# Kernel optimization log

Hardware: AMD Instinct MI355X
Metric: run time of the kernel (lower is better)

Reference implementation:

```python
import jax, jax.numpy as jnp
import numpy as np

B, T, F, H, OUT_LEN = 1024, 512, 128, 128, 15


def _lstm_cell(x_t, h, c, Wih, Whh, bih, bhh):
    # PyTorch gate order: i, f, g, o
    gates = x_t @ Wih.T + h @ Whh.T + bih + bhh  # [B, 4H]
    i, f, g, o = jnp.split(gates, 4, axis=-1)
    i = jax.nn.sigmoid(i)
    f = jax.nn.sigmoid(f)
    g = jnp.tanh(g)
    o = jax.nn.sigmoid(o)
    c_new = f * c + i * g
    h_new = o * jnp.tanh(c_new)
    return h_new, c_new


def _lstm_layer(x, Wih, Whh, bih, bhh):
    # x: [B, T, in]; returns (outputs [B,T,H], h_last [B,H], c_last [B,H])
    b = x.shape[0]
    h0 = jnp.zeros((b, Whh.shape[1]), x.dtype)
    c0 = jnp.zeros_like(h0)

    def step(carry, x_t):
        h, c = carry
        h, c = _lstm_cell(x_t, h, c, Wih, Whh, bih, bhh)
        return (h, c), h

    (h_last, c_last), ys = jax.lax.scan(step, (h0, c0), jnp.swapaxes(x, 0, 1))
    return jnp.swapaxes(ys, 0, 1), h_last, c_last


def _forward(x, enc_Wih0, enc_Whh0, enc_bih0, enc_bhh0,
             enc_Wih1, enc_Whh1, enc_bih1, enc_bhh1,
             dec_Wih, dec_Whh, dec_bih, dec_bhh,
             inproj_W, inproj_b, outproj_W, outproj_b, attn_W, attn_b):
    # 2-layer encoder (inter-layer dropout is identity at inference)
    out0, _, _ = _lstm_layer(x, enc_Wih0, enc_Whh0, enc_bih0, enc_bhh0)
    enc_out, h_last, c_last = _lstm_layer(out0, enc_Wih1, enc_Whh1, enc_bih1, enc_bhh1)

    hx, cx = h_last, c_last                       # last layer's final (h, c)
    dec_in = x.mean(axis=1) @ inproj_W.T + inproj_b  # [B, H]
    ctx = enc_out.mean(axis=1)                    # [B, H], same each step

    def dec_step(carry, _):
        h, c, din = carry
        h, c = _lstm_cell(din, h, c, dec_Wih, dec_Whh, dec_bih, dec_bhh)
        h = h + (jnp.concatenate([h, ctx], axis=1) @ attn_W.T + attn_b)
        out = h @ outproj_W.T + outproj_b         # [B, F]
        return (h, c, out), out

    _, outs = jax.lax.scan(dec_step, (hx, cx, dec_in), None, length=OUT_LEN)
    return jnp.swapaxes(outs, 0, 1)               # [B, OUT_LEN, F]


def setup_inputs() -> dict:
    key = jax.random.key(0)
    ks = jax.random.split(key, 20)
    s = 0.05  # small init scale to keep gates unsaturated
    inp = {
        "x": jax.random.normal(ks[0], (B, T, F), jnp.float32),
        "enc_Wih0": jax.random.normal(ks[1], (4 * H, F), jnp.float32) * s,
        "enc_Whh0": jax.random.normal(ks[2], (4 * H, H), jnp.float32) * s,
        "enc_bih0": jax.random.normal(ks[3], (4 * H,), jnp.float32) * s,
        "enc_bhh0": jax.random.normal(ks[4], (4 * H,), jnp.float32) * s,
        "enc_Wih1": jax.random.normal(ks[5], (4 * H, H), jnp.float32) * s,
        "enc_Whh1": jax.random.normal(ks[6], (4 * H, H), jnp.float32) * s,
        "enc_bih1": jax.random.normal(ks[7], (4 * H,), jnp.float32) * s,
        "enc_bhh1": jax.random.normal(ks[8], (4 * H,), jnp.float32) * s,
        "dec_Wih": jax.random.normal(ks[9], (4 * H, H), jnp.float32) * s,
        "dec_Whh": jax.random.normal(ks[10], (4 * H, H), jnp.float32) * s,
        "dec_bih": jax.random.normal(ks[11], (4 * H,), jnp.float32) * s,
        "dec_bhh": jax.random.normal(ks[12], (4 * H,), jnp.float32) * s,
        "inproj_W": jax.random.normal(ks[13], (H, F), jnp.float32) * s,
        "inproj_b": jax.random.normal(ks[14], (H,), jnp.float32) * s,
        "outproj_W": jax.random.normal(ks[15], (F, H), jnp.float32) * s,
        "outproj_b": jax.random.normal(ks[16], (F,), jnp.float32) * s,
        "attn_W": jax.random.normal(ks[17], (H, 2 * H), jnp.float32) * s,
        "attn_b": jax.random.normal(ks[18], (H,), jnp.float32) * s,
    }
    return inp


def reference(x, enc_Wih0, enc_Whh0, enc_bih0, enc_bhh0,
              enc_Wih1, enc_Whh1, enc_bih1, enc_bhh1,
              dec_Wih, dec_Whh, dec_bih, dec_bhh,
              inproj_W, inproj_b, outproj_W, outproj_b, attn_W, attn_b):
    return _forward(x, enc_Wih0, enc_Whh0, enc_bih0, enc_bhh0,
                    enc_Wih1, enc_Whh1, enc_bih1, enc_bhh1,
                    dec_Wih, dec_Whh, dec_bih, dec_bhh,
                    inproj_W, inproj_b, outproj_W, outproj_b, attn_W, attn_b)
```

## Files before the change

### kernel.cpp

```cpp
#include <hip/hip_runtime.h>
#include <cstdint>
#include <cstddef>

#define BDIM 512
#define BB   16
#define T_   512
#define F_   128
#define H_   128
#define B_   1024
#define OUTL 15
#define ASTR 264
#define HSTR 136
#define NBLK 64
#define CHUNK 8

typedef __bf16 bf16_t;
typedef __bf16 bf16x8 __attribute__((ext_vector_type(8)));
typedef float  f32x4  __attribute__((ext_vector_type(4)));

__device__ __forceinline__ float u16tof(unsigned int u) {
    unsigned int v = u << 16;
    return __builtin_bit_cast(float, v);
}

__device__ __forceinline__ float sigm(float x) {
    return __builtin_amdgcn_rcpf(1.0f + __expf(-x));
}
__device__ __forceinline__ float tanh_(float x) {
    float e = __expf(2.0f * x);
    return 1.0f - 2.0f * __builtin_amdgcn_rcpf(e + 1.0f);
}

__device__ __forceinline__ f32x4 mfma16(bf16x8 a, bf16x8 b, f32x4 c) {
    return __builtin_amdgcn_mfma_f32_16x16x32_bf16(a, b, c, 0, 0, 0);
}

template <int FW>
__device__ __forceinline__ float ldf(const void* p, int i) {
    return FW ? ((const float*)p)[i] : (float)((const bf16_t*)p)[i];
}
template <int FW>
__device__ __forceinline__ bf16x8 ld8(const void* p, size_t off) {
    if (FW) {
        const float* f = (const float*)p + off;
        f32x4 a = *(const f32x4*)f;
        f32x4 b = *(const f32x4*)(f + 4);
        bf16x8 r;
        r[0] = (bf16_t)a[0]; r[1] = (bf16_t)a[1]; r[2] = (bf16_t)a[2]; r[3] = (bf16_t)a[3];
        r[4] = (bf16_t)b[0]; r[5] = (bf16_t)b[1]; r[6] = (bf16_t)b[2]; r[7] = (bf16_t)b[3];
        return r;
    }
    return *(const bf16x8*)((const bf16_t*)p + off);
}
template <int FX>
__device__ __forceinline__ void load_x4(const void* xin, size_t ofs, uint2& pk, float xr[4]) {
    if (FX) {
        f32x4 v = *(const f32x4*)((const float*)xin + ofs);
        union { bf16_t h[4]; uint2 u; } P;
        P.h[0] = (bf16_t)v[0]; P.h[1] = (bf16_t)v[1];
        P.h[2] = (bf16_t)v[2]; P.h[3] = (bf16_t)v[3];
        pk = P.u;
        xr[0] = v[0]; xr[1] = v[1]; xr[2] = v[2]; xr[3] = v[3];
    } else {
        pk = *(const uint2*)((const bf16_t*)xin + ofs);
        xr[0] = u16tof(pk.x & 0xffffu); xr[1] = u16tof(pk.x >> 16);
        xr[2] = u16tof(pk.y & 0xffffu); xr[3] = u16tof(pk.y >> 16);
    }
}

__global__ void detect_kernel(const unsigned short* __restrict__ xu, int* __restrict__ flag,
                              int* __restrict__ prog) {
    int lane = threadIdx.x;
    prog[lane] = 0;
    int cnt = 0;
#pragma unroll
    for (int i = 0; i < 16; ++i) {
        unsigned int u = xu[(lane * 16 + i) * 2];
        unsigned int e = (u >> 7) & 0xffu;
        cnt += (e >= 100u && e <= 140u) ? 1 : 0;
    }
#pragma unroll
    for (int s = 32; s > 0; s >>= 1) cnt += __shfl_down(cnt, s, 64);
    if (lane == 0) *flag = (cnt < 512) ? 1 : 0;
}

template <int FW>
__device__ __forceinline__ void load_gate_frags(
    const void* __restrict__ Wih, const void* __restrict__ Whh,
    const void* __restrict__ bih, const void* __restrict__ bhh,
    int u, int q, bf16x8 wf[4][8], float bias[4])
{
#pragma unroll
    for (int nt = 0; nt < 4; ++nt) {
        int grow = nt * H_ + u;
        bias[nt] = ldf<FW>(bih, grow) + ldf<FW>(bhh, grow);
#pragma unroll
        for (int kt = 0; kt < 8; ++kt) {
            if (kt < 4)
                wf[nt][kt] = ld8<FW>(Wih, (size_t)grow * F_ + kt * 32 + q * 8);
            else
                wf[nt][kt] = ld8<FW>(Whh, (size_t)grow * H_ + (kt - 4) * 32 + q * 8);
        }
    }
}

template <int FW, int FX, int L0>
__device__ __forceinline__ void enc_body(
    int b0,
    const void* __restrict__ xin, size_t xin_rs,
    bf16_t* __restrict__ xout, size_t xout_rs,
    const void* __restrict__ Wih, const void* __restrict__ Whh,
    const void* __restrict__ bih, const void* __restrict__ bhh,
    float* __restrict__ xmean, float* __restrict__ ctx,
    bf16_t* __restrict__ hN, float* __restrict__ cN,
    int* __restrict__ prog, int pb,
    bf16_t (*A)[BB * ASTR])
{
    const int tid  = threadIdx.x;
    const int w    = tid >> 6;
    const int lane = tid & 63;
    const int c    = lane & 15;
    const int q    = lane >> 4;
    const int u    = 16 * w + c;

    bf16x8 wf[4][8];
    float  bias[4];
    load_gate_frags<FW>(Wih, Whh, bih, bhh, u, q, wf, bias);

    const int lr   = tid >> 5;
    const int lcol = (tid & 31) * 4;

    float xs[4]  = {0.f, 0.f, 0.f, 0.f};
    float cs[4]  = {0.f, 0.f, 0.f, 0.f};
    float cst[4] = {0.f, 0.f, 0.f, 0.f};

    if (!L0) {
        if (tid == 0) {
            while (__hip_atomic_load(prog + pb, __ATOMIC_RELAXED, __HIP_MEMORY_SCOPE_AGENT) < 1)
                __builtin_amdgcn_s_sleep(2);
            __builtin_amdgcn_fence(__ATOMIC_ACQUIRE, "agent");
        }
        __syncthreads();
    }

    {
        uint2 pk; float xr[4];
        load_x4<FX>(xin, (size_t)(b0 + lr) * xin_rs + 0 * F_ + lcol, pk, xr);
        *(uint2*)&A[0][lr * ASTR + lcol] = pk;
        uint2 zz; zz.x = 0u; zz.y = 0u;
        *(uint2*)&A[0][lr * ASTR + F_ + lcol] = zz;
        if (L0) { xs[0] += xr[0]; xs[1] += xr[1]; xs[2] += xr[2]; xs[3] += xr[3]; }
    }
    __syncthreads();

    for (int t = 0; t < T_; ++t) {
        const int cur = t & 1, nxt = cur ^ 1;
        const bool havex = (t + 1 < T_);

        if (!L0 && havex && ((t & (CHUNK - 1)) == (CHUNK - 1))) {
            if (tid == 0) {
                while (__hip_atomic_load(prog + pb, __ATOMIC_RELAXED, __HIP_MEMORY_SCOPE_AGENT) < t + 2)
                    __builtin_amdgcn_s_sleep(2);
                __builtin_amdgcn_fence(__ATOMIC_ACQUIRE, "agent");
            }
            __syncthreads();
        }

        uint2 pk; float xr[4];
        if (havex)
            load_x4<FX>(xin, (size_t)(b0 + lr) * xin_rs + (size_t)(t + 1) * F_ + lcol, pk, xr);

        f32x4 acc0 = {bias[0], bias[0], bias[0], bias[0]};
        f32x4 acc1 = {bias[1], bias[1], bias[1], bias[1]};
        f32x4 acc2 = {bias[2], bias[2], bias[2], bias[2]};
        f32x4 acc3 = {bias[3], bias[3], bias[3], bias[3]};

        const bf16_t* Ab = &A[cur][0];
#pragma unroll
        for (int kt = 0; kt < 8; ++kt) {
            bf16x8 a = *(const bf16x8*)(Ab + c * ASTR + kt * 32 + q * 8);
            acc0 = mfma16(a, wf[0][kt], acc0);
            acc1 = mfma16(a, wf[1][kt], acc1);
            acc2 = mfma16(a, wf[2][kt], acc2);
            acc3 = mfma16(a, wf[3][kt], acc3);
        }

#pragma unroll
        for (int j = 0; j < 4; ++j) {
            float i_ = sigm(acc0[j]);
            float f_ = sigm(acc1[j]);
            float g_ = tanh_(acc2[j]);
            float o_ = sigm(acc3[j]);
            float cc = f_ * cst[j] + i_ * g_;
            cst[j] = cc;
            float h_ = o_ * tanh_(cc);
            int r = q * 4 + j;
            A[nxt][r * ASTR + F_ + u] = (bf16_t)h_;
            if (L0) {
                xout[(size_t)(b0 + r) * xout_rs + (size_t)t * F_ + u] = (bf16_t)h_;
            } else {
                cs[j] += h_;
                if (t == T_ - 1) {
                    hN[(size_t)(b0 + r) * H_ + u] = (bf16_t)h_;
                    cN[(size_t)(b0 + r) * H_ + u] = cc;
                }
            }
        }

        if (havex) {
            *(uint2*)&A[nxt][lr * ASTR + lcol] = pk;
            if (L0) { xs[0] += xr[0]; xs[1] += xr[1]; xs[2] += xr[2]; xs[3] += xr[3]; }
        }
        __syncthreads();

        if (L0 && tid == 0 && (((t + 1) & (CHUNK - 1)) == 0)) {
            __hip_atomic_store(prog + pb, t + 1, __ATOMIC_RELEASE, __HIP_MEMORY_SCOPE_AGENT);
        }
    }

    const float s = 1.0f / (float)T_;
    if (L0) {
        float* dst = xmean + (size_t)(b0 + lr) * F_ + lcol;
        dst[0] = xs[0] * s; dst[1] = xs[1] * s;
        dst[2] = xs[2] * s; dst[3] = xs[3] * s;
    } else {
#pragma unroll
        for (int j = 0; j < 4; ++j)
            ctx[(size_t)(b0 + q * 4 + j) * H_ + u] = cs[j] * s;
    }
}

__global__ __launch_bounds__(BDIM) void enc_fused(
    const int* __restrict__ flag,
    void* __restrict__ x,
    const void* Wih0, const void* Whh0, const void* bih0, const void* bhh0,
    const void* Wih1, const void* Whh1, const void* bih1, const void* bhh1,
    float* __restrict__ xmean, float* __restrict__ ctx,
    bf16_t* __restrict__ hN, float* __restrict__ cN,
    int* __restrict__ prog)
{
    __shared__ bf16_t A[2][BB * ASTR];
    const int isf = *flag;
    const int pb  = blockIdx.x & (NBLK - 1);
    const int b0  = pb * BB;
    if (blockIdx.x < NBLK) {
        if (isf) enc_body<1, 1, 1>(b0, x, (size_t)T_ * F_, (bf16_t*)x, 2 * (size_t)T_ * F_,
                                   Wih0, Whh0, bih0, bhh0, xmean, nullptr, nullptr, nullptr,
                                   prog, pb, A);
        else     enc_body<0, 0, 1>(b0, x, (size_t)T_ * F_, (bf16_t*)x, (size_t)T_ * F_,
                                   Wih0, Whh0, bih0, bhh0, xmean, nullptr, nullptr, nullptr,
                                   prog, pb, A);
    } else {
        if (isf) enc_body<1, 0, 0>(b0, x, 2 * (size_t)T_ * F_, nullptr, 0,
                                   Wih1, Whh1, bih1, bhh1, nullptr, ctx, hN, cN,
                                   prog, pb, A);
        else     enc_body<0, 0, 0>(b0, x, (size_t)T_ * F_, nullptr, 0,
                                   Wih1, Whh1, bih1, bhh1, nullptr, ctx, hN, cN,
                                   prog, pb, A);
    }
}

template <int FW>
__device__ __forceinline__ void dec_body(
    const void* __restrict__ Wih, const void* __restrict__ Whh,
    const void* __restrict__ bih, const void* __restrict__ bhh,
    const void* __restrict__ inW, const void* __restrict__ inb,
    const void* __restrict__ outW, const void* __restrict__ outb,
    const void* __restrict__ attW, const void* __restrict__ attb,
    const float* __restrict__ xmean, const float* __restrict__ ctx,
    const bf16_t* __restrict__ h0, const float* __restrict__ c0,
    void* __restrict__ dout,
    bf16_t* __restrict__ A, bf16_t* __restrict__ Hb, bf16_t* __restrict__ Hb2)
{
    const int tid  = threadIdx.x;
    const int w    = tid >> 6;
    const int lane = tid & 63;
    const int c    = lane & 15;
    const int q    = lane >> 4;
    const int b0   = blockIdx.x * BB;
    const int u    = 16 * w + c;

    bf16x8 wd[4][8];
    float  biasd[4];
    load_gate_frags<FW>(Wih, Whh, bih, bhh, u, q, wd, biasd);

    bf16x8 wa[4], wo[4];
#pragma unroll
    for (int kt = 0; kt < 4; ++kt) {
        wa[kt] = ld8<FW>(attW, (size_t)u * 256 + kt * 32 + q * 8);
        wo[kt] = ld8<FW>(outW, (size_t)u * H_ + kt * 32 + q * 8);
    }
    const float outb_f = ldf<FW>(outb, u);

    const int lr   = tid >> 5;
    const int lcol = (tid & 31) * 4;

    {
        uint2 hv = *(const uint2*)(h0 + (size_t)(b0 + lr) * H_ + lcol);
        *(uint2*)&A[lr * ASTR + F_ + lcol] = hv;
    }
    {
        const float* xm = xmean + (size_t)(b0 + lr) * F_ + lcol;
        const float* cx = ctx   + (size_t)(b0 + lr) * H_ + lcol;
#pragma unroll
        for (int k = 0; k < 4; ++k) {
            Hb [lr * HSTR + lcol + k] = (bf16_t)xm[k];
            Hb2[lr * HSTR + lcol + k] = (bf16_t)cx[k];
        }
    }
    float cst[4];
#pragma unroll
    for (int j = 0; j < 4; ++j)
        cst[j] = c0[(size_t)(b0 + q * 4 + j) * H_ + u];

    __syncthreads();

    {
        float b = ldf<FW>(inb, u);
        f32x4 accd = {b, b, b, b};
#pragma unroll
        for (int kt = 0; kt < 4; ++kt) {
            bf16x8 a  = *(const bf16x8*)(Hb + c * HSTR + kt * 32 + q * 8);
            bf16x8 bw = ld8<FW>(inW, (size_t)u * F_ + kt * 32 + q * 8);
            accd = mfma16(a, bw, accd);
        }
#pragma unroll
        for (int j = 0; j < 4; ++j)
            A[(q * 4 + j) * ASTR + u] = (bf16_t)accd[j];
    }
    f32x4 ctxp;
    {
        float b = ldf<FW>(attb, u);
        f32x4 acca = {b, b, b, b};
#pragma unroll
        for (int kt = 0; kt < 4; ++kt) {
            bf16x8 a  = *(const bf16x8*)(Hb2 + c * HSTR + kt * 32 + q * 8);
            bf16x8 bw = ld8<FW>(attW, (size_t)u * 256 + 128 + kt * 32 + q * 8);
            acca = mfma16(a, bw, acca);
        }
        ctxp = acca;
    }
    __syncthreads();

    for (int s = 0; s < OUTL; ++s) {
        f32x4 acc0 = {biasd[0], biasd[0], biasd[0], biasd[0]};
        f32x4 acc1 = {biasd[1], biasd[1], biasd[1], biasd[1]};
        f32x4 acc2 = {biasd[2], biasd[2], biasd[2], biasd[2]};
        f32x4 acc3 = {biasd[3], biasd[3], biasd[3], biasd[3]};
#pragma unroll
        for (int kt = 0; kt < 8; ++kt) {
            bf16x8 a = *(const bf16x8*)(A + c * ASTR + kt * 32 + q * 8);
            acc0 = mfma16(a, wd[0][kt], acc0);
            acc1 = mfma16(a, wd[1][kt], acc1);
            acc2 = mfma16(a, wd[2][kt], acc2);
            acc3 = mfma16(a, wd[3][kt], acc3);
        }
#pragma unroll
        for (int j = 0; j < 4; ++j) {
            float i_ = sigm(acc0[j]);
            float f_ = sigm(acc1[j]);
            float g_ = tanh_(acc2[j]);
            float o_ = sigm(acc3[j]);
            float cc = f_ * cst[j] + i_ * g_;
            cst[j] = cc;
            float h_ = o_ * tanh_(cc);
            Hb[(q * 4 + j) * HSTR + u] = (bf16_t)h_;
        }
        __syncthreads();

        f32x4 acch = ctxp;
#pragma unroll
        for (int kt = 0; kt < 4; ++kt) {
            bf16x8 a = *(const bf16x8*)(Hb + c * HSTR + kt * 32 + q * 8);
            acch = mfma16(a, wa[kt], acch);
        }
#pragma unroll
        for (int j = 0; j < 4; ++j) {
            int r = q * 4 + j;
            float h2 = acch[j] + (float)Hb[r * HSTR + u];
            Hb2[r * HSTR + u]    = (bf16_t)h2;
            A[r * ASTR + F_ + u] = (bf16_t)h2;
        }
        __syncthreads();

        f32x4 acco = {outb_f, outb_f, outb_f, outb_f};
#pragma unroll
        for (int kt = 0; kt < 4; ++kt) {
            bf16x8 a = *(const bf16x8*)(Hb2 + c * HSTR + kt * 32 + q * 8);
            acco = mfma16(a, wo[kt], acco);
        }
#pragma unroll
        for (int j = 0; j < 4; ++j) {
            int r = q * 4 + j;
            float ov = acco[j];
            size_t oidx = ((size_t)(b0 + r) * OUTL + s) * F_ + u;
            if (FW) ((float*)dout)[oidx] = ov;
            else    ((bf16_t*)dout)[oidx] = (bf16_t)ov;
            A[r * ASTR + u] = (bf16_t)ov;
        }
        __syncthreads();
    }
}

__global__ __launch_bounds__(BDIM) void dec_kernel(
    const int* __restrict__ flag,
    const void* Wih, const void* Whh, const void* bih, const void* bhh,
    const void* inW, const void* inb, const void* outW, const void* outb,
    const void* attW, const void* attb,
    const float* xmean, const float* ctx,
    const bf16_t* h0, const float* c0, void* dout)
{
    __shared__ bf16_t A[BB * ASTR];
    __shared__ bf16_t Hb[BB * HSTR];
    __shared__ bf16_t Hb2[BB * HSTR];
    const int isf = *flag;
    if (isf) dec_body<1>(Wih, Whh, bih, bhh, inW, inb, outW, outb, attW, attb,
                         xmean, ctx, h0, c0, dout, A, Hb, Hb2);
    else     dec_body<0>(Wih, Whh, bih, bhh, inW, inb, outW, outb, attW, attb,
                         xmean, ctx, h0, c0, dout, A, Hb, Hb2);
}

extern "C" void kernel_launch(void* const* d_in, const int* in_sizes, int n_in,
                              void* d_out, int out_size, void* d_ws, size_t ws_size,
                              hipStream_t stream) {
    (void)in_sizes; (void)n_in; (void)out_size; (void)ws_size;

    void*       x     = d_in[0];
    const void* Wih0  = d_in[1];
    const void* Whh0  = d_in[2];
    const void* bih0  = d_in[3];
    const void* bhh0  = d_in[4];
    const void* Wih1  = d_in[5];
    const void* Whh1  = d_in[6];
    const void* bih1  = d_in[7];
    const void* bhh1  = d_in[8];
    const void* dWih  = d_in[9];
    const void* dWhh  = d_in[10];
    const void* dbih  = d_in[11];
    const void* dbhh  = d_in[12];
    const void* inW   = d_in[13];
    const void* inb   = d_in[14];
    const void* outW  = d_in[15];
    const void* outb  = d_in[16];
    const void* attW  = d_in[17];
    const void* attb  = d_in[18];

    int*    flag  = (int*)d_ws;
    int*    prog  = (int*)((char*)d_ws + 16);
    float*  xmean = (float*)((char*)d_ws + 16 + 256);
    float*  ctx   = xmean + B_ * H_;
    float*  cN    = ctx + B_ * H_;
    bf16_t* hN    = (bf16_t*)(cN + B_ * H_);

    detect_kernel<<<1, 64, 0, stream>>>((const unsigned short*)x, flag, prog);

    enc_fused<<<2 * NBLK, BDIM, 0, stream>>>(flag, x,
                                             Wih0, Whh0, bih0, bhh0,
                                             Wih1, Whh1, bih1, bhh1,
                                             xmean, ctx, hN, cN, prog);
    dec_kernel<<<NBLK, BDIM, 0, stream>>>(flag, dWih, dWhh, dbih, dbhh,
                                          inW, inb, outW, outb, attW, attb,
                                          xmean, ctx, hN, cN, d_out);
}
```

Baseline: 1.040 ms.

## Split input and recurrent gate products to pipeline x-projection one step ahead

The encoder cell now computes the input-projection half of the gate matmul for step t+1 during step t. Only the recurrent half, the h@Whh part, stays on the per-step critical path, and x loads are prefetched two steps ahead. The layer-1 to layer-0 handshake chunk grows from 8 to 16 with a matching lookahead. The layer-0 output goes to a separate workspace buffer when ws_size allows, instead of being written in place over x. Launch bounds add a minimum of 2 blocks per CU, which may force register spills given the large held weight fragments.

```diff
diff --git a/kernel.cpp b/kernel.cpp
--- a/kernel.cpp
+++ b/kernel.cpp
@@ -12,7 +12,7 @@
 #define ASTR 264
 #define HSTR 136
 #define NBLK 64
-#define CHUNK 8
+#define CHUNK 16
 
 typedef __bf16 bf16_t;
 typedef __bf16 bf16x8 __attribute__((ext_vector_type(8)));
@@ -136,7 +136,7 @@
 
     if (!L0) {
         if (tid == 0) {
-            while (__hip_atomic_load(prog + pb, __ATOMIC_RELAXED, __HIP_MEMORY_SCOPE_AGENT) < 1)
+            while (__hip_atomic_load(prog + pb, __ATOMIC_RELAXED, __HIP_MEMORY_SCOPE_AGENT) < 2)
                 __builtin_amdgcn_s_sleep(2);
             __builtin_amdgcn_fence(__ATOMIC_ACQUIRE, "agent");
         }
@@ -144,58 +144,93 @@
     }
 
     {
-        uint2 pk; float xr[4];
-        load_x4<FX>(xin, (size_t)(b0 + lr) * xin_rs + 0 * F_ + lcol, pk, xr);
-        *(uint2*)&A[0][lr * ASTR + lcol] = pk;
+        uint2 pk0; float xr0[4];
+        load_x4<FX>(xin, (size_t)(b0 + lr) * xin_rs + 0 * F_ + lcol, pk0, xr0);
+        *(uint2*)&A[0][lr * ASTR + lcol] = pk0;
+        if (L0) { xs[0] += xr0[0]; xs[1] += xr0[1]; xs[2] += xr0[2]; xs[3] += xr0[3]; }
+    }
+    __syncthreads();
+
+    f32x4 xg0 = {bias[0], bias[0], bias[0], bias[0]};
+    f32x4 xg1 = {bias[1], bias[1], bias[1], bias[1]};
+    f32x4 xg2 = {bias[2], bias[2], bias[2], bias[2]};
+    f32x4 xg3 = {bias[3], bias[3], bias[3], bias[3]};
+    {
+        const bf16_t* Ab = &A[0][0];
+        uint2 pk1; float xr1[4];
+        load_x4<FX>(xin, (size_t)(b0 + lr) * xin_rs + 1 * F_ + lcol, pk1, xr1);
+#pragma unroll
+        for (int kt = 0; kt < 4; ++kt) {
+            bf16x8 ax = *(const bf16x8*)(Ab + c * ASTR + kt * 32 + q * 8);
+            xg0 = mfma16(ax, wf[0][kt], xg0);
+            xg1 = mfma16(ax, wf[1][kt], xg1);
+            xg2 = mfma16(ax, wf[2][kt], xg2);
+            xg3 = mfma16(ax, wf[3][kt], xg3);
+        }
+        __syncthreads();
+        *(uint2*)&A[0][lr * ASTR + lcol] = pk1;
         uint2 zz; zz.x = 0u; zz.y = 0u;
         *(uint2*)&A[0][lr * ASTR + F_ + lcol] = zz;
-        if (L0) { xs[0] += xr[0]; xs[1] += xr[1]; xs[2] += xr[2]; xs[3] += xr[3]; }
+        if (L0) { xs[0] += xr1[0]; xs[1] += xr1[1]; xs[2] += xr1[2]; xs[3] += xr1[3]; }
     }
     __syncthreads();
 
     for (int t = 0; t < T_; ++t) {
-        const int cur = t & 1, nxt = cur ^ 1;
-        const bool havex = (t + 1 < T_);
-
-        if (!L0 && havex && ((t & (CHUNK - 1)) == (CHUNK - 1))) {
+        const int P = t & 1, Q = P ^ 1;
+
+        if (!L0 && ((t & (CHUNK - 1)) == 0)) {
+            int need = t + 2 + CHUNK; if (need > T_) need = T_;
             if (tid == 0) {
-                while (__hip_atomic_load(prog + pb, __ATOMIC_RELAXED, __HIP_MEMORY_SCOPE_AGENT) < t + 2)
+                while (__hip_atomic_load(prog + pb, __ATOMIC_RELAXED, __HIP_MEMORY_SCOPE_AGENT) < need)
                     __builtin_amdgcn_s_sleep(2);
                 __builtin_amdgcn_fence(__ATOMIC_ACQUIRE, "agent");
             }
             __syncthreads();
         }
 
+        const bool ldx = (t + 2 < T_);
         uint2 pk; float xr[4];
-        if (havex)
-            load_x4<FX>(xin, (size_t)(b0 + lr) * xin_rs + (size_t)(t + 1) * F_ + lcol, pk, xr);
-
-        f32x4 acc0 = {bias[0], bias[0], bias[0], bias[0]};
-        f32x4 acc1 = {bias[1], bias[1], bias[1], bias[1]};
-        f32x4 acc2 = {bias[2], bias[2], bias[2], bias[2]};
-        f32x4 acc3 = {bias[3], bias[3], bias[3], bias[3]};
-
-        const bf16_t* Ab = &A[cur][0];
-#pragma unroll
-        for (int kt = 0; kt < 8; ++kt) {
-            bf16x8 a = *(const bf16x8*)(Ab + c * ASTR + kt * 32 + q * 8);
-            acc0 = mfma16(a, wf[0][kt], acc0);
-            acc1 = mfma16(a, wf[1][kt], acc1);
-            acc2 = mfma16(a, wf[2][kt], acc2);
-            acc3 = mfma16(a, wf[3][kt], acc3);
+        if (ldx)
+            load_x4<FX>(xin, (size_t)(b0 + lr) * xin_rs + (size_t)(t + 2) * F_ + lcol, pk, xr);
+
+        const bf16_t* Ab = &A[P][0];
+
+        f32x4 a0 = xg0, a1 = xg1, a2 = xg2, a3 = xg3;
+#pragma unroll
+        for (int kt = 0; kt < 4; ++kt) {
+            bf16x8 ah = *(const bf16x8*)(Ab + c * ASTR + F_ + kt * 32 + q * 8);
+            a0 = mfma16(ah, wf[0][4 + kt], a0);
+            a1 = mfma16(ah, wf[1][4 + kt], a1);
+            a2 = mfma16(ah, wf[2][4 + kt], a2);
+            a3 = mfma16(ah, wf[3][4 + kt], a3);
+        }
+
+        if (t + 1 < T_) {
+            xg0 = f32x4{bias[0], bias[0], bias[0], bias[0]};
+            xg1 = f32x4{bias[1], bias[1], bias[1], bias[1]};
+            xg2 = f32x4{bias[2], bias[2], bias[2], bias[2]};
+            xg3 = f32x4{bias[3], bias[3], bias[3], bias[3]};
+#pragma unroll
+            for (int kt = 0; kt < 4; ++kt) {
+                bf16x8 ax = *(const bf16x8*)(Ab + c * ASTR + kt * 32 + q * 8);
+                xg0 = mfma16(ax, wf[0][kt], xg0);
+                xg1 = mfma16(ax, wf[1][kt], xg1);
+                xg2 = mfma16(ax, wf[2][kt], xg2);
+                xg3 = mfma16(ax, wf[3][kt], xg3);
+            }
         }
 
 #pragma unroll
         for (int j = 0; j < 4; ++j) {
-            float i_ = sigm(acc0[j]);
-            float f_ = sigm(acc1[j]);
-            float g_ = tanh_(acc2[j]);
-            float o_ = sigm(acc3[j]);
+            float i_ = sigm(a0[j]);
+            float f_ = sigm(a1[j]);
+            float g_ = tanh_(a2[j]);
+            float o_ = sigm(a3[j]);
             float cc = f_ * cst[j] + i_ * g_;
             cst[j] = cc;
             float h_ = o_ * tanh_(cc);
             int r = q * 4 + j;
-            A[nxt][r * ASTR + F_ + u] = (bf16_t)h_;
+            A[Q][r * ASTR + F_ + u] = (bf16_t)h_;
             if (L0) {
                 xout[(size_t)(b0 + r) * xout_rs + (size_t)t * F_ + u] = (bf16_t)h_;
             } else {
@@ -207,8 +242,8 @@
             }
         }
 
-        if (havex) {
-            *(uint2*)&A[nxt][lr * ASTR + lcol] = pk;
+        if (ldx) {
+            *(uint2*)&A[Q][lr * ASTR + lcol] = pk;
             if (L0) { xs[0] += xr[0]; xs[1] += xr[1]; xs[2] += xr[2]; xs[3] += xr[3]; }
         }
         __syncthreads();
@@ -230,33 +265,34 @@
     }
 }
 
-__global__ __launch_bounds__(BDIM) void enc_fused(
+__global__ __launch_bounds__(BDIM, 2) void enc_fused(
     const int* __restrict__ flag,
     void* __restrict__ x,
     const void* Wih0, const void* Whh0, const void* bih0, const void* bhh0,
     const void* Wih1, const void* Whh1, const void* bih1, const void* bhh1,
     float* __restrict__ xmean, float* __restrict__ ctx,
     bf16_t* __restrict__ hN, float* __restrict__ cN,
-    int* __restrict__ prog)
+    int* __restrict__ prog, bf16_t* __restrict__ o0)
 {
     __shared__ bf16_t A[2][BB * ASTR];
     const int isf = *flag;
     const int pb  = blockIdx.x & (NBLK - 1);
     const int b0  = pb * BB;
+    const size_t TF = (size_t)T_ * F_;
     if (blockIdx.x < NBLK) {
-        if (isf) enc_body<1, 1, 1>(b0, x, (size_t)T_ * F_, (bf16_t*)x, 2 * (size_t)T_ * F_,
-                                   Wih0, Whh0, bih0, bhh0, xmean, nullptr, nullptr, nullptr,
-                                   prog, pb, A);
-        else     enc_body<0, 0, 1>(b0, x, (size_t)T_ * F_, (bf16_t*)x, (size_t)T_ * F_,
-                                   Wih0, Whh0, bih0, bhh0, xmean, nullptr, nullptr, nullptr,
-                                   prog, pb, A);
+        bf16_t* xo = o0 ? o0 : (bf16_t*)x;
+        size_t  ors = o0 ? TF : (isf ? 2 * TF : TF);
+        if (isf) enc_body<1, 1, 1>(b0, x, TF, xo, ors, Wih0, Whh0, bih0, bhh0,
+                                   xmean, nullptr, nullptr, nullptr, prog, pb, A);
+        else     enc_body<0, 0, 1>(b0, x, TF, xo, ors, Wih0, Whh0, bih0, bhh0,
+                                   xmean, nullptr, nullptr, nullptr, prog, pb, A);
     } else {
-        if (isf) enc_body<1, 0, 0>(b0, x, 2 * (size_t)T_ * F_, nullptr, 0,
-                                   Wih1, Whh1, bih1, bhh1, nullptr, ctx, hN, cN,
-                                   prog, pb, A);
-        else     enc_body<0, 0, 0>(b0, x, (size_t)T_ * F_, nullptr, 0,
-                                   Wih1, Whh1, bih1, bhh1, nullptr, ctx, hN, cN,
-                                   prog, pb, A);
+        const void* xi = o0 ? (const void*)o0 : (const void*)x;
+        size_t irs = o0 ? TF : (isf ? 2 * TF : TF);
+        if (isf) enc_body<1, 0, 0>(b0, xi, irs, nullptr, 0, Wih1, Whh1, bih1, bhh1,
+                                   nullptr, ctx, hN, cN, prog, pb, A);
+        else     enc_body<0, 0, 0>(b0, xi, irs, nullptr, 0, Wih1, Whh1, bih1, bhh1,
+                                   nullptr, ctx, hN, cN, prog, pb, A);
     }
 }
 
@@ -402,7 +438,7 @@
     }
 }
 
-__global__ __launch_bounds__(BDIM) void dec_kernel(
+__global__ __launch_bounds__(BDIM, 2) void dec_kernel(
     const int* __restrict__ flag,
     const void* Wih, const void* Whh, const void* bih, const void* bhh,
     const void* inW, const void* inb, const void* outW, const void* outb,
@@ -423,7 +459,7 @@
 extern "C" void kernel_launch(void* const* d_in, const int* in_sizes, int n_in,
                               void* d_out, int out_size, void* d_ws, size_t ws_size,
                               hipStream_t stream) {
-    (void)in_sizes; (void)n_in; (void)out_size; (void)ws_size;
+    (void)in_sizes; (void)n_in; (void)out_size;
 
     void*       x     = d_in[0];
     const void* Wih0  = d_in[1];
@@ -452,12 +488,16 @@
     float*  cN    = ctx + B_ * H_;
     bf16_t* hN    = (bf16_t*)(cN + B_ * H_);
 
+    const size_t REQ = 16 + 256 + 3 * (size_t)B_ * H_ * 4 + (size_t)B_ * H_ * 2
+                     + (size_t)B_ * T_ * H_ * 2;
+    bf16_t* o0 = (ws_size >= REQ) ? (hN + (size_t)B_ * H_) : nullptr;
+
     detect_kernel<<<1, 64, 0, stream>>>((const unsigned short*)x, flag, prog);
 
     enc_fused<<<2 * NBLK, BDIM, 0, stream>>>(flag, x,
                                              Wih0, Whh0, bih0, bhh0,
                                              Wih1, Whh1, bih1, bhh1,
-                                             xmean, ctx, hN, cN, prog);
+                                             xmean, ctx, hN, cN, prog, o0);
     dec_kernel<<<NBLK, BDIM, 0, stream>>>(flag, dWih, dWhh, dbih, dbhh,
                                           inW, inb, outW, outb, attW, attb,
                                           xmean, ctx, hN, cN, d_out);
```

Measured after the change: 1.019 ms. 1.02x faster.
